# Kernel tuning notes

Hardware: AMD Instinct MI355X
Metric: run time of the kernel (lower is better)

## Reference

```python
import jax, jax.numpy as jnp
import numpy as np

TOKEN_DIM = 256
N_HEADS = 8
HEAD_DIM = TOKEN_DIM // N_HEADS


def setup_inputs() -> dict:
    key = jax.random.key(0)
    ks = jax.random.split(key, 10)
    B, S, D = 4, 2048, TOKEN_DIM
    s = 1.0 / np.sqrt(D)
    return {
        "x": jax.random.normal(ks[0], (B, S, D), dtype=jnp.float32),
        "Wq": jax.random.uniform(ks[1], (D, D), jnp.float32, -s, s),
        "bq": jax.random.uniform(ks[2], (D,), jnp.float32, -s, s),
        "Wk": jax.random.uniform(ks[3], (D, D), jnp.float32, -s, s),
        "bk": jax.random.uniform(ks[4], (D,), jnp.float32, -s, s),
        "Wv": jax.random.uniform(ks[5], (D, D), jnp.float32, -s, s),
        "bv": jax.random.uniform(ks[6], (D,), jnp.float32, -s, s),
        "Wo": jax.random.uniform(ks[7], (D, D), jnp.float32, -s, s),
        "bo": jax.random.uniform(ks[8], (D,), jnp.float32, -s, s),
        "head_scale": jnp.ones((N_HEADS,), dtype=jnp.float32),
    }


def reference(x, Wq, bq, Wk, bk, Wv, bv, Wo, bo, head_scale):
    B, S, D = x.shape
    H, Hd = N_HEADS, HEAD_DIM
    scale = jnp.asarray(np.sqrt(Hd), x.dtype)

    def split_heads(t):
        return t.reshape(B, S, H, Hd).transpose(0, 2, 1, 3)  # (B,H,S,Hd)

    Q = split_heads(x @ Wq.T + bq)
    K = split_heads(x @ Wk.T + bk)
    V = split_heads(x @ Wv.T + bv)

    scores = jnp.einsum("bhsd,bhtd->bhst", Q, K) / scale  # (B,H,S,S)
    attn = jax.nn.softmax(scores, axis=-1)
    attn_scaled = attn * head_scale[None, :, None, None]
    Hctx = jnp.einsum("bhst,bhtd->bhsd", attn_scaled, V)
    Hctx = Hctx.transpose(0, 2, 1, 3).reshape(B, S, D)
    return Hctx @ Wo.T + bo
```

## Files before the change

### kernel.cpp

```cpp
#include <hip/hip_runtime.h>
#include <hip/hip_bf16.h>
#include <math.h>

#define B_ 4
#define S_ 2048
#define D_ 256
#define H_ 8
#define HD_ 32

typedef __attribute__((ext_vector_type(8))) short short8;
typedef __attribute__((ext_vector_type(4))) short short4v;
typedef __attribute__((ext_vector_type(4))) float floatx4;
typedef unsigned short ushort_t;
typedef unsigned int uint_t;

typedef union { unsigned u[2]; short4v v4; } PkU;

#define CVT_PK(DST, LO, HI) \
  asm volatile("v_cvt_pk_bf16_f32 %0, %1, %2" : "=v"(DST) : "v"(LO), "v"(HI))

#define MFMA16(ACC, A, B) \
  asm volatile("v_mfma_f32_16x16x16_bf16 %0, %1, %2, %0" : "+v"(ACC) : "v"(A), "v"(B))

__device__ __forceinline__ ushort_t f2bf(float f) {
  union { float f; unsigned u; } v; v.f = f;
  unsigned u = v.u;
  unsigned r = (u + 0x7FFFu + ((u >> 16) & 1u)) >> 16;
  return (ushort_t)r;
}

__global__ __launch_bounds__(256)
void cvt_all(const float* __restrict__ x,
             const float* __restrict__ wq, const float* __restrict__ wk,
             const float* __restrict__ wv, const float* __restrict__ wo,
             ushort_t* __restrict__ xb,
             ushort_t* __restrict__ wqb, ushort_t* __restrict__ wkb,
             ushort_t* __restrict__ wvb, ushort_t* __restrict__ wob)
{
  const int b = blockIdx.x;
  const float4* s; uint2* d; int i;
  if (b < 2048) {
    s = (const float4*)x; d = (uint2*)xb; i = b * 256 + threadIdx.x;
  } else {
    int r = b - 2048; int mm = r >> 6;
    s = (const float4*)(mm == 0 ? wq : mm == 1 ? wk : mm == 2 ? wv : wo);
    d = (uint2*)(mm == 0 ? wqb : mm == 1 ? wkb : mm == 2 ? wvb : wob);
    i = (r & 63) * 256 + threadIdx.x;
  }
  float4 f = s[i];
  uint2 o;
  CVT_PK(o.x, f.x, f.y);
  CVT_PK(o.y, f.z, f.w);
  d[i] = o;
}

__global__ __launch_bounds__(256)
void proj_qkv(const ushort_t* __restrict__ xb,
              const ushort_t* __restrict__ wq, const ushort_t* __restrict__ wk, const ushort_t* __restrict__ wv,
              const float* __restrict__ bq, const float* __restrict__ bk, const float* __restrict__ bv,
              ushort_t* __restrict__ qout, ushort_t* __restrict__ kout, ushort_t* __restrict__ vout)
{
  __shared__ __align__(16) ushort_t W_lds[64 * 264];

  const int z = blockIdx.z;
  const ushort_t* wb = (z == 0) ? wq : (z == 1) ? wk : wv;
  const float* bias  = (z == 0) ? bq : (z == 1) ? bk : bv;

  const int t = threadIdx.x;
  const int l = t & 63;
  const int w = t >> 6;
  const int row0 = blockIdx.y * 128 + w * 16;
  const int col0 = blockIdx.x * 64;
  const int lr = l & 15, lg = l >> 4, lk = lg * 8;

  {
    const ushort_t* wsrc = wb + (col0 + (t >> 2)) * D_ + (t & 3) * 64;
    ushort_t* wdst = &W_lds[(t >> 2) * 264 + (t & 3) * 64];
#pragma unroll
    for (int i = 0; i < 8; ++i)
      *(uint4*)(wdst + i * 8) = *(const uint4*)(wsrc + i * 8);
  }
  __syncthreads();

  floatx4 acc[2][4] = {};
  const ushort_t* arow0 = xb + (row0 + lr) * D_ + lk;
  const ushort_t* arow1 = xb + (row0 + 64 + lr) * D_ + lk;
#pragma unroll
  for (int kk = 0; kk < D_; kk += 32) {
    short8 a0 = *(const short8*)(arow0 + kk);
    short8 a1 = *(const short8*)(arow1 + kk);
#pragma unroll
    for (int j = 0; j < 4; ++j) {
      short8 b = *(const short8*)&W_lds[(j * 16 + lr) * 264 + kk + lk];
      acc[0][j] = __builtin_amdgcn_mfma_f32_16x16x32_bf16(a0, b, acc[0][j], 0, 0, 0);
      acc[1][j] = __builtin_amdgcn_mfma_f32_16x16x32_bf16(a1, b, acc[1][j], 0, 0, 0);
    }
  }

  if (z == 2) {
#pragma unroll
    for (int rs = 0; rs < 2; ++rs)
#pragma unroll
      for (int j = 0; j < 4; ++j) {
        int c = col0 + j * 16 + lr;
        float bv_ = bias[c];
        int hh = c >> 5, d = c & 31;
        int i0 = row0 + rs * 64 + lg * 4;
        int bb = i0 >> 11, s0 = i0 & 2047;
        uint2 pv;
        CVT_PK(pv.x, acc[rs][j][0] + bv_, acc[rs][j][1] + bv_);
        CVT_PK(pv.y, acc[rs][j][2] + bv_, acc[rs][j][3] + bv_);
        *(uint2*)&vout[(((size_t)(bb * H_ + hh)) * HD_ + d) * S_ + s0] = pv;
      }
  } else {
    ushort_t* dst = (z == 0) ? qout : kout;
    const float qscale = (z == 0) ? 0.25503486f : 1.0f;
#pragma unroll
    for (int rs = 0; rs < 2; ++rs)
#pragma unroll
      for (int j = 0; j < 4; ++j) {
        int c = col0 + j * 16 + lr;
        float bv_ = bias[c];
        int hh = c >> 5, d = c & 31;
#pragma unroll
        for (int rp = 0; rp < 2; ++rp) {
          int i = row0 + rs * 64 + lg * 4 + rp * 2;
          int bb = i >> 11, s = i & 2047;
          uint_t pr;
          CVT_PK(pr, (acc[rs][j][rp*2] + bv_) * qscale, (acc[rs][j][rp*2+1] + bv_) * qscale);
          size_t b0 = ((size_t)(bb * H_ + hh) * S_ + s) * HD_ + d;
          dst[b0]       = (ushort_t)(pr & 0xffffu);
          dst[b0 + HD_] = (ushort_t)(pr >> 16);
        }
      }
  }
}

__global__ __launch_bounds__(512)
void attn_kernel(const ushort_t* __restrict__ qb, const ushort_t* __restrict__ kb,
                 const ushort_t* __restrict__ vtb, const float* __restrict__ head_scale,
                 ushort_t* __restrict__ hb)
{
  __shared__ __align__(16) ushort_t K_lds[2][128 * 40];
  __shared__ __align__(16) ushort_t Vt_lds[2][32 * 140];

  const int tid = threadIdx.x;
  const int l = tid & 63;
  const int w = tid >> 6;
  const int f = blockIdx.y * 16 + blockIdx.x;
  const int qt = f >> 5;
  const int bh = (f & 7) * 4 + ((f >> 3) & 3);
  const int lr = l & 15;
  const int lg = l >> 4;

  const ushort_t* qp  = qb  + (size_t)bh * S_ * HD_;
  const ushort_t* kp  = kb  + (size_t)bh * S_ * HD_;
  const ushort_t* vtp = vtb + (size_t)bh * S_ * HD_;

  const int q0 = qt * 128 + w * 16;
  short8 qfrag = *(const short8*)(qp + (q0 + lr) * HD_ + lg * 8);

  floatx4 oA = {}, oB = {}, oL = {};

  const int kr = tid >> 2, kc = (tid & 3) * 8;
  const int vr = tid >> 4, vc = (tid & 15) * 8;

  const short4v ones4 = {0x3F80, 0x3F80, 0x3F80, 0x3F80};
  const floatx4 zero4 = {0.f, 0.f, 0.f, 0.f};

  uint4 kreg = *(const uint4*)(kp + kr * HD_ + kc);
  uint4 vreg = *(const uint4*)(vtp + vr * S_ + vc);
  *(uint4*)&K_lds[0][kr * 40 + kc] = kreg;
  {
    ushort_t* vd = &Vt_lds[0][vr * 140 + vc];
    *(uint2*)(vd)     = make_uint2(vreg.x, vreg.y);
    *(uint2*)(vd + 4) = make_uint2(vreg.z, vreg.w);
  }

  int cur = 0;
  for (int t0 = 0; t0 < S_; t0 += 128) {
    __syncthreads();

    const int tn = (t0 + 128) & (S_ - 1);
    kreg = *(const uint4*)(kp + (tn + kr) * HD_ + kc);
    vreg = *(const uint4*)(vtp + vr * S_ + tn + vc);

    floatx4 sv[8];
#pragma unroll
    for (int s = 0; s < 8; ++s) {
      short8 kf = *(const short8*)&K_lds[cur][(s * 16 + lr) * 40 + lg * 8];
      sv[s] = __builtin_amdgcn_mfma_f32_16x16x32_bf16(kf, qfrag, zero4, 0, 0, 0);
    }

    PkU pk[8];
    __builtin_amdgcn_s_setprio(1);
#pragma unroll
    for (int s = 0; s < 2; ++s) {
      sv[s][0] = __builtin_amdgcn_exp2f(sv[s][0]);
      sv[s][1] = __builtin_amdgcn_exp2f(sv[s][1]);
      sv[s][2] = __builtin_amdgcn_exp2f(sv[s][2]);
      sv[s][3] = __builtin_amdgcn_exp2f(sv[s][3]);
    }
    CVT_PK(pk[0].u[0], sv[0][0], sv[0][1]);
    CVT_PK(pk[0].u[1], sv[0][2], sv[0][3]);
    CVT_PK(pk[1].u[0], sv[1][0], sv[1][1]);
    CVT_PK(pk[1].u[1], sv[1][2], sv[1][3]);
#pragma unroll
    for (int s = 0; s < 8; ++s) {
      const int cb = s * 16 + lg * 4;
      short4v a0 = *(const short4v*)&Vt_lds[cur][lr * 140 + cb];
      short4v a1 = *(const short4v*)&Vt_lds[cur][(16 + lr) * 140 + cb];
      MFMA16(oA, a0, pk[s].v4);
      MFMA16(oB, a1, pk[s].v4);
      MFMA16(oL, ones4, pk[s].v4);
      if (s + 2 < 8) {
        sv[s+2][0] = __builtin_amdgcn_exp2f(sv[s+2][0]);
        sv[s+2][1] = __builtin_amdgcn_exp2f(sv[s+2][1]);
        sv[s+2][2] = __builtin_amdgcn_exp2f(sv[s+2][2]);
        sv[s+2][3] = __builtin_amdgcn_exp2f(sv[s+2][3]);
        CVT_PK(pk[s+2].u[0], sv[s+2][0], sv[s+2][1]);
        CVT_PK(pk[s+2].u[1], sv[s+2][2], sv[s+2][3]);
      }
    }
    __builtin_amdgcn_s_setprio(0);

    *(uint4*)&K_lds[cur ^ 1][kr * 40 + kc] = kreg;
    {
      ushort_t* vd = &Vt_lds[cur ^ 1][vr * 140 + vc];
      *(uint2*)(vd)     = make_uint2(vreg.x, vreg.y);
      *(uint2*)(vd + 4) = make_uint2(vreg.z, vreg.w);
    }
    cur ^= 1;
  }

  asm volatile("s_nop 7\n\ts_nop 7" :::);
  const int bb = bh >> 3, hh = bh & 7;
  float inv = head_scale[hh] / oL[0];
  const int sq = q0 + lr;
  size_t base = ((size_t)(bb * S_ + sq)) * D_ + hh * HD_;
  uint2 w0, w1;
  CVT_PK(w0.x, oA[0] * inv, oA[1] * inv);
  CVT_PK(w0.y, oA[2] * inv, oA[3] * inv);
  CVT_PK(w1.x, oB[0] * inv, oB[1] * inv);
  CVT_PK(w1.y, oB[2] * inv, oB[3] * inv);
  *(uint2*)&hb[base + lg * 4] = w0;
  *(uint2*)&hb[base + 16 + lg * 4] = w1;
}

__global__ __launch_bounds__(256)
void proj_out(const ushort_t* __restrict__ hbm, const ushort_t* __restrict__ wo,
              const float* __restrict__ bo, float* __restrict__ out)
{
  __shared__ __align__(16) ushort_t W_lds[64 * 264];

  const int t = threadIdx.x;
  const int l = t & 63;
  const int w = t >> 6;
  const int row0 = blockIdx.y * 128 + w * 16;
  const int col0 = blockIdx.x * 64;
  const int lr = l & 15, lg = l >> 4, lk = lg * 8;

  {
    const ushort_t* wsrc = wo + (col0 + (t >> 2)) * D_ + (t & 3) * 64;
    ushort_t* wdst = &W_lds[(t >> 2) * 264 + (t & 3) * 64];
#pragma unroll
    for (int i = 0; i < 8; ++i)
      *(uint4*)(wdst + i * 8) = *(const uint4*)(wsrc + i * 8);
  }
  __syncthreads();

  floatx4 acc[2][4] = {};
  const ushort_t* arow0 = hbm + (row0 + lr) * D_ + lk;
  const ushort_t* arow1 = hbm + (row0 + 64 + lr) * D_ + lk;
#pragma unroll
  for (int kk = 0; kk < D_; kk += 32) {
    short8 a0 = *(const short8*)(arow0 + kk);
    short8 a1 = *(const short8*)(arow1 + kk);
#pragma unroll
    for (int j = 0; j < 4; ++j) {
      short8 b = *(const short8*)&W_lds[(j * 16 + lr) * 264 + kk + lk];
      acc[0][j] = __builtin_amdgcn_mfma_f32_16x16x32_bf16(a0, b, acc[0][j], 0, 0, 0);
      acc[1][j] = __builtin_amdgcn_mfma_f32_16x16x32_bf16(a1, b, acc[1][j], 0, 0, 0);
    }
  }
#pragma unroll
  for (int rs = 0; rs < 2; ++rs)
#pragma unroll
    for (int j = 0; j < 4; ++j) {
      int c = col0 + j * 16 + lr;
      float bias = bo[c];
#pragma unroll
      for (int r = 0; r < 4; ++r) {
        int i = row0 + rs * 64 + lg * 4 + r;
        out[(size_t)i * D_ + c] = acc[rs][j][r] + bias;
      }
    }
}

extern "C" void kernel_launch(void* const* d_in, const int* in_sizes, int n_in,
                              void* d_out, int out_size, void* d_ws, size_t ws_size,
                              hipStream_t stream) {
  (void)in_sizes; (void)n_in; (void)out_size; (void)ws_size;
  const float* x  = (const float*)d_in[0];
  const float* Wq = (const float*)d_in[1];
  const float* bq = (const float*)d_in[2];
  const float* Wk = (const float*)d_in[3];
  const float* bk = (const float*)d_in[4];
  const float* Wv = (const float*)d_in[5];
  const float* bv = (const float*)d_in[6];
  const float* Wo = (const float*)d_in[7];
  const float* bo = (const float*)d_in[8];
  const float* hs = (const float*)d_in[9];

  char* ws = (char*)d_ws;
  ushort_t* xb  = (ushort_t*)ws;
  ushort_t* wqb = (ushort_t*)(ws + 4 * 1024 * 1024);
  ushort_t* wkb = wqb + 65536;
  ushort_t* wvb = wkb + 65536;
  ushort_t* wob = wvb + 65536;
  ushort_t* qb  = wob + 65536;
  ushort_t* kbb = qb + 2097152;
  ushort_t* vbb = kbb + 2097152;
  ushort_t* hbb = xb;

  cvt_all<<<2304, 256, 0, stream>>>(x, Wq, Wk, Wv, Wo, xb, wqb, wkb, wvb, wob);
  proj_qkv<<<dim3(4, 64, 3), 256, 0, stream>>>(xb, wqb, wkb, wvb, bq, bk, bv, qb, kbb, vbb);
  attn_kernel<<<dim3(16, 32), 512, 0, stream>>>(qb, kbb, vbb, hs, hbb);
  proj_out<<<dim3(4, 64), 256, 0, stream>>>(hbb, wob, bo, (float*)d_out);
}
```

Before: 58.36 us.

## Split attention key range in two and add combine kernel

Splits each attention block's key/value sweep into two halves, doubling the grid from 512 to 1024 blocks. Each half writes unnormalized fp32 partial outputs and row sums to workspace. A new combine kernel adds the halves, normalizes with head_scale, and writes bf16 context. The aim is better occupancy of the GPU's compute units, paid for by extra fp32 partial traffic and one more kernel launch.

```diff
diff --git a/kernel.cpp b/kernel.cpp
--- a/kernel.cpp
+++ b/kernel.cpp
@@ -138,8 +138,8 @@
 
 __global__ __launch_bounds__(512)
 void attn_kernel(const ushort_t* __restrict__ qb, const ushort_t* __restrict__ kb,
-                 const ushort_t* __restrict__ vtb, const float* __restrict__ head_scale,
-                 ushort_t* __restrict__ hb)
+                 const ushort_t* __restrict__ vtb,
+                 float* __restrict__ opart, float* __restrict__ lpart)
 {
   __shared__ __align__(16) ushort_t K_lds[2][128 * 40];
   __shared__ __align__(16) ushort_t Vt_lds[2][32 * 140];
@@ -147,9 +147,11 @@
   const int tid = threadIdx.x;
   const int l = tid & 63;
   const int w = tid >> 6;
-  const int f = blockIdx.y * 16 + blockIdx.x;
-  const int qt = f >> 5;
-  const int bh = (f & 7) * 4 + ((f >> 3) & 3);
+  const int f = blockIdx.y * 32 + blockIdx.x;
+  const int half = f >> 9;
+  const int rem = f & 511;
+  const int qt = rem >> 5;
+  const int bh = (rem & 7) * 4 + ((rem >> 3) & 3);
   const int lr = l & 15;
   const int lg = l >> 4;
 
@@ -168,8 +170,11 @@
   const short4v ones4 = {0x3F80, 0x3F80, 0x3F80, 0x3F80};
   const floatx4 zero4 = {0.f, 0.f, 0.f, 0.f};
 
-  uint4 kreg = *(const uint4*)(kp + kr * HD_ + kc);
-  uint4 vreg = *(const uint4*)(vtp + vr * S_ + vc);
+  const int t_begin = half << 10;
+  const int t_end   = t_begin + 1024;
+
+  uint4 kreg = *(const uint4*)(kp + (t_begin + kr) * HD_ + kc);
+  uint4 vreg = *(const uint4*)(vtp + vr * S_ + t_begin + vc);
   *(uint4*)&K_lds[0][kr * 40 + kc] = kreg;
   {
     ushort_t* vd = &Vt_lds[0][vr * 140 + vc];
@@ -178,10 +183,10 @@
   }
 
   int cur = 0;
-  for (int t0 = 0; t0 < S_; t0 += 128) {
+  for (int t0 = t_begin; t0 < t_end; t0 += 128) {
     __syncthreads();
 
-    const int tn = (t0 + 128) & (S_ - 1);
+    int tn = t0 + 128; if (tn == t_end) tn = t_begin;
     kreg = *(const uint4*)(kp + (tn + kr) * HD_ + kc);
     vreg = *(const uint4*)(vtp + vr * S_ + tn + vc);
 
@@ -234,17 +239,32 @@
   }
 
   asm volatile("s_nop 7\n\ts_nop 7" :::);
-  const int bb = bh >> 3, hh = bh & 7;
-  float inv = head_scale[hh] / oL[0];
-  const int sq = q0 + lr;
-  size_t base = ((size_t)(bb * S_ + sq)) * D_ + hh * HD_;
-  uint2 w0, w1;
-  CVT_PK(w0.x, oA[0] * inv, oA[1] * inv);
-  CVT_PK(w0.y, oA[2] * inv, oA[3] * inv);
-  CVT_PK(w1.x, oB[0] * inv, oB[1] * inv);
-  CVT_PK(w1.y, oB[2] * inv, oB[3] * inv);
-  *(uint2*)&hb[base + lg * 4] = w0;
-  *(uint2*)&hb[base + 16 + lg * 4] = w1;
+  const size_t prow = ((size_t)(half * 32 + bh)) * S_ + q0 + lr;
+  *(floatx4*)&opart[prow * 32 + lg * 4]      = oA;
+  *(floatx4*)&opart[prow * 32 + 16 + lg * 4] = oB;
+  if (lg == 0) lpart[prow] = oL[0];
+}
+
+__global__ __launch_bounds__(256)
+void combine(const float* __restrict__ opart, const float* __restrict__ lpart,
+             const float* __restrict__ head_scale, ushort_t* __restrict__ hb)
+{
+  const int idx = blockIdx.x * 256 + threadIdx.x;
+  const int row = idx >> 2;
+  const int c8  = (idx & 3) * 8;
+  const float* o0 = opart + (size_t)row * 32 + c8;
+  const float* o1 = opart + ((size_t)(65536 + row)) * 32 + c8;
+  const float lsum = lpart[row] + lpart[65536 + row];
+  const int bh = row >> 11, hh = bh & 7, bb = bh >> 3, s = row & 2047;
+  const float inv = head_scale[hh] / lsum;
+  float4 a0 = *(const float4*)o0, b0 = *(const float4*)(o0 + 4);
+  float4 a1 = *(const float4*)o1, b1 = *(const float4*)(o1 + 4);
+  uint4 w;
+  CVT_PK(w.x, (a0.x + a1.x) * inv, (a0.y + a1.y) * inv);
+  CVT_PK(w.y, (a0.z + a1.z) * inv, (a0.w + a1.w) * inv);
+  CVT_PK(w.z, (b0.x + b1.x) * inv, (b0.y + b1.y) * inv);
+  CVT_PK(w.w, (b0.z + b1.z) * inv, (b0.w + b1.w) * inv);
+  *(uint4*)&hb[((size_t)(bb * S_ + s)) * D_ + hh * HD_ + c8] = w;
 }
 
 __global__ __launch_bounds__(256)
@@ -321,10 +341,13 @@
   ushort_t* qb  = wob + 65536;
   ushort_t* kbb = qb + 2097152;
   ushort_t* vbb = kbb + 2097152;
+  float* opart  = (float*)(vbb + 2097152);
+  float* lpart  = opart + 4194304;
   ushort_t* hbb = xb;
 
   cvt_all<<<2304, 256, 0, stream>>>(x, Wq, Wk, Wv, Wo, xb, wqb, wkb, wvb, wob);
   proj_qkv<<<dim3(4, 64, 3), 256, 0, stream>>>(xb, wqb, wkb, wvb, bq, bk, bv, qb, kbb, vbb);
-  attn_kernel<<<dim3(16, 32), 512, 0, stream>>>(qb, kbb, vbb, hs, hbb);
+  attn_kernel<<<dim3(32, 32), 512, 0, stream>>>(qb, kbb, vbb, opart, lpart);
+  combine<<<1024, 256, 0, stream>>>(opart, lpart, hs, hbb);
   proj_out<<<dim3(4, 64), 256, 0, stream>>>(hbb, wob, bo, (float*)d_out);
 }
```

After: 63.75 us. 1.09x slower.

## Fuse Q/K/V projections into one block that reuses x tile from registers

Applied to the files above, without the earlier changes.

The QKV projection kernel now launches one block per row/column tile instead of three. Each block loads its x activation rows into registers once and loops over the Q, K and V weight matrices, restaging each into LDS and reusing the same A operands. This cuts redundant global reads of x, but it reduces the grid from 768 to 256 blocks and serialises the three projections within a block, which raises register pressure and lowers parallelism.

```diff
diff --git a/kernel.cpp b/kernel.cpp
--- a/kernel.cpp
+++ b/kernel.cpp
@@ -62,9 +62,8 @@
 {
   __shared__ __align__(16) ushort_t W_lds[64 * 264];
 
-  const int z = blockIdx.z;
-  const ushort_t* wb = (z == 0) ? wq : (z == 1) ? wk : wv;
-  const float* bias  = (z == 0) ? bq : (z == 1) ? bk : bv;
+  const ushort_t* wbs[3] = {wq, wk, wv};
+  const float*    bis[3] = {bq, bk, bv};
 
   const int t = threadIdx.x;
   const int l = t & 63;
@@ -73,66 +72,78 @@
   const int col0 = blockIdx.x * 64;
   const int lr = l & 15, lg = l >> 4, lk = lg * 8;
 
+  short8 a0[8], a1[8];
   {
-    const ushort_t* wsrc = wb + (col0 + (t >> 2)) * D_ + (t & 3) * 64;
-    ushort_t* wdst = &W_lds[(t >> 2) * 264 + (t & 3) * 64];
-#pragma unroll
-    for (int i = 0; i < 8; ++i)
-      *(uint4*)(wdst + i * 8) = *(const uint4*)(wsrc + i * 8);
-  }
-  __syncthreads();
-
-  floatx4 acc[2][4] = {};
-  const ushort_t* arow0 = xb + (row0 + lr) * D_ + lk;
-  const ushort_t* arow1 = xb + (row0 + 64 + lr) * D_ + lk;
-#pragma unroll
-  for (int kk = 0; kk < D_; kk += 32) {
-    short8 a0 = *(const short8*)(arow0 + kk);
-    short8 a1 = *(const short8*)(arow1 + kk);
-#pragma unroll
-    for (int j = 0; j < 4; ++j) {
-      short8 b = *(const short8*)&W_lds[(j * 16 + lr) * 264 + kk + lk];
-      acc[0][j] = __builtin_amdgcn_mfma_f32_16x16x32_bf16(a0, b, acc[0][j], 0, 0, 0);
-      acc[1][j] = __builtin_amdgcn_mfma_f32_16x16x32_bf16(a1, b, acc[1][j], 0, 0, 0);
-    }
-  }
-
-  if (z == 2) {
-#pragma unroll
-    for (int rs = 0; rs < 2; ++rs)
+    const ushort_t* arow0 = xb + (row0 + lr) * D_ + lk;
+    const ushort_t* arow1 = xb + (row0 + 64 + lr) * D_ + lk;
+#pragma unroll
+    for (int kk = 0; kk < 8; ++kk) {
+      a0[kk] = *(const short8*)(arow0 + kk * 32);
+      a1[kk] = *(const short8*)(arow1 + kk * 32);
+    }
+  }
+
+#pragma unroll
+  for (int z = 0; z < 3; ++z) {
+    if (z > 0) __syncthreads();
+    {
+      const ushort_t* wsrc = wbs[z] + (col0 + (t >> 2)) * D_ + (t & 3) * 64;
+      ushort_t* wdst = &W_lds[(t >> 2) * 264 + (t & 3) * 64];
+#pragma unroll
+      for (int i = 0; i < 8; ++i)
+        *(uint4*)(wdst + i * 8) = *(const uint4*)(wsrc + i * 8);
+    }
+    __syncthreads();
+
+    floatx4 acc[2][4] = {};
+#pragma unroll
+    for (int kk = 0; kk < 8; ++kk) {
 #pragma unroll
       for (int j = 0; j < 4; ++j) {
-        int c = col0 + j * 16 + lr;
-        float bv_ = bias[c];
-        int hh = c >> 5, d = c & 31;
-        int i0 = row0 + rs * 64 + lg * 4;
-        int bb = i0 >> 11, s0 = i0 & 2047;
-        uint2 pv;
-        CVT_PK(pv.x, acc[rs][j][0] + bv_, acc[rs][j][1] + bv_);
-        CVT_PK(pv.y, acc[rs][j][2] + bv_, acc[rs][j][3] + bv_);
-        *(uint2*)&vout[(((size_t)(bb * H_ + hh)) * HD_ + d) * S_ + s0] = pv;
+        short8 b = *(const short8*)&W_lds[(j * 16 + lr) * 264 + kk * 32 + lk];
+        acc[0][j] = __builtin_amdgcn_mfma_f32_16x16x32_bf16(a0[kk], b, acc[0][j], 0, 0, 0);
+        acc[1][j] = __builtin_amdgcn_mfma_f32_16x16x32_bf16(a1[kk], b, acc[1][j], 0, 0, 0);
       }
-  } else {
-    ushort_t* dst = (z == 0) ? qout : kout;
-    const float qscale = (z == 0) ? 0.25503486f : 1.0f;
-#pragma unroll
-    for (int rs = 0; rs < 2; ++rs)
-#pragma unroll
-      for (int j = 0; j < 4; ++j) {
-        int c = col0 + j * 16 + lr;
-        float bv_ = bias[c];
-        int hh = c >> 5, d = c & 31;
-#pragma unroll
-        for (int rp = 0; rp < 2; ++rp) {
-          int i = row0 + rs * 64 + lg * 4 + rp * 2;
-          int bb = i >> 11, s = i & 2047;
-          uint_t pr;
-          CVT_PK(pr, (acc[rs][j][rp*2] + bv_) * qscale, (acc[rs][j][rp*2+1] + bv_) * qscale);
-          size_t b0 = ((size_t)(bb * H_ + hh) * S_ + s) * HD_ + d;
-          dst[b0]       = (ushort_t)(pr & 0xffffu);
-          dst[b0 + HD_] = (ushort_t)(pr >> 16);
+    }
+
+    const float* bias = bis[z];
+    if (z == 2) {
+#pragma unroll
+      for (int rs = 0; rs < 2; ++rs)
+#pragma unroll
+        for (int j = 0; j < 4; ++j) {
+          int c = col0 + j * 16 + lr;
+          float bv_ = bias[c];
+          int hh = c >> 5, d = c & 31;
+          int i0 = row0 + rs * 64 + lg * 4;
+          int bb = i0 >> 11, s0 = i0 & 2047;
+          uint2 pv;
+          CVT_PK(pv.x, acc[rs][j][0] + bv_, acc[rs][j][1] + bv_);
+          CVT_PK(pv.y, acc[rs][j][2] + bv_, acc[rs][j][3] + bv_);
+          *(uint2*)&vout[(((size_t)(bb * H_ + hh)) * HD_ + d) * S_ + s0] = pv;
         }
-      }
+    } else {
+      ushort_t* dst = (z == 0) ? qout : kout;
+      const float qscale = (z == 0) ? 0.25503486f : 1.0f;
+#pragma unroll
+      for (int rs = 0; rs < 2; ++rs)
+#pragma unroll
+        for (int j = 0; j < 4; ++j) {
+          int c = col0 + j * 16 + lr;
+          float bv_ = bias[c];
+          int hh = c >> 5, d = c & 31;
+#pragma unroll
+          for (int rp = 0; rp < 2; ++rp) {
+            int i = row0 + rs * 64 + lg * 4 + rp * 2;
+            int bb = i >> 11, s = i & 2047;
+            uint_t pr;
+            CVT_PK(pr, (acc[rs][j][rp*2] + bv_) * qscale, (acc[rs][j][rp*2+1] + bv_) * qscale);
+            size_t b0 = ((size_t)(bb * H_ + hh) * S_ + s) * HD_ + d;
+            dst[b0]       = (ushort_t)(pr & 0xffffu);
+            dst[b0 + HD_] = (ushort_t)(pr >> 16);
+          }
+        }
+    }
   }
 }
 
@@ -324,7 +335,7 @@
   ushort_t* hbb = xb;
 
   cvt_all<<<2304, 256, 0, stream>>>(x, Wq, Wk, Wv, Wo, xb, wqb, wkb, wvb, wob);
-  proj_qkv<<<dim3(4, 64, 3), 256, 0, stream>>>(xb, wqb, wkb, wvb, bq, bk, bv, qb, kbb, vbb);
+  proj_qkv<<<dim3(4, 64), 256, 0, stream>>>(xb, wqb, wkb, wvb, bq, bk, bv, qb, kbb, vbb);
   attn_kernel<<<dim3(16, 32), 512, 0, stream>>>(qb, kbb, vbb, hs, hbb);
   proj_out<<<dim3(4, 64), 256, 0, stream>>>(hbb, wob, bo, (float*)d_out);
 }
```

New measurement: 59.61 us. 2.1% more time.
